# Kernel optimization log

Hardware: AMD Instinct MI355X
Metric: run time of the kernel (lower is better)

## Reference

```python
import jax, jax.numpy as jnp
import numpy as np

B, H, W = 8, 256, 256
NF = 64          # num_feat
E = 12           # num_expert
D = NF * 4       # token dim = 256
CD = D * E       # expanded dim = 3072


def _lrelu(x):
    return jnp.where(x >= 0, x, 0.2 * x)


def _conv(x, w, stride, pad):
    return jax.lax.conv_general_dilated(
        x, w, (stride, stride), [(pad, pad), (pad, pad)],
        dimension_numbers=('NCHW', 'OIHW', 'NCHW'))


def _bn(x, g, b):
    # training-mode BatchNorm2d: batch statistics over (N, H, W)
    m = jnp.mean(x, axis=(0, 2, 3), keepdims=True)
    v = jnp.var(x, axis=(0, 2, 3), keepdims=True)
    xn = (x - m) * jax.lax.rsqrt(v + 1e-5)
    return xn * g[None, :, None, None] + b[None, :, None, None]


def setup_inputs() -> dict:
    key = jax.random.key(0)
    ks = jax.random.split(key, 16)
    s = 0.05
    d = {}
    d['x'] = jax.random.normal(ks[0], (B, 3, H, W), jnp.float32)
    d['conv0_w'] = jax.random.normal(ks[1], (NF, 3, 3, 3)) * s
    d['conv0_b'] = jnp.zeros((NF,))
    d['conv1_w'] = jax.random.normal(ks[2], (NF, NF, 4, 4)) * s
    d['bn1_g'] = jnp.ones((NF,)); d['bn1_b'] = jnp.zeros((NF,))
    d['conv2_w'] = jax.random.normal(ks[3], (2 * NF, NF, 3, 3)) * s
    d['bn2_g'] = jnp.ones((2 * NF,)); d['bn2_b'] = jnp.zeros((2 * NF,))
    d['conv3_w'] = jax.random.normal(ks[4], (2 * NF, 2 * NF, 4, 4)) * s
    d['bn3_g'] = jnp.ones((2 * NF,)); d['bn3_b'] = jnp.zeros((2 * NF,))
    d['conv4_w'] = jax.random.normal(ks[5], (4 * NF, 2 * NF, 3, 3)) * s
    d['bn4_g'] = jnp.ones((4 * NF,)); d['bn4_b'] = jnp.zeros((4 * NF,))
    d['conv5_w'] = jax.random.normal(ks[6], (4 * NF, 4 * NF, 3, 3)) * s
    d['bn5_g'] = jnp.ones((4 * NF,)); d['bn5_b'] = jnp.zeros((4 * NF,))
    d['conv6_w'] = jax.random.normal(ks[7], (4 * NF, 4 * NF, 3, 3)) * s
    d['bn6_g'] = jnp.ones((4 * NF,)); d['bn6_b'] = jnp.zeros((4 * NF,))
    d['w_gating'] = jax.random.normal(ks[8], (D, E))          # torch.randn init
    d['body_w'] = jax.random.normal(ks[9], (D, CD)) * s       # Linear(c_dim, c_dim*blocks)
    d['body_b'] = jnp.zeros((CD,))
    d['ortho_w'] = jax.random.normal(ks[10], (1, 1, CD))      # OrthorTransform weight
    d['cls_w1'] = jax.random.normal(ks[11], (D, NF // 2)) * s # shared classifier
    d['cls_b1'] = jnp.zeros((NF // 2,))
    d['cls_w2'] = jax.random.normal(ks[12], (NF // 2, 1)) * s
    d['cls_b2'] = jnp.zeros((1,))
    return d


def reference(x, conv0_w, conv0_b, conv1_w, bn1_g, bn1_b, conv2_w, bn2_g, bn2_b,
              conv3_w, bn3_g, bn3_b, conv4_w, bn4_g, bn4_b, conv5_w, bn5_g, bn5_b,
              conv6_w, bn6_g, bn6_b, w_gating, body_w, body_b, ortho_w,
              cls_w1, cls_b1, cls_w2, cls_b2):
    # --- FE conv stack ---
    h = _lrelu(_conv(x, conv0_w, 1, 1) + conv0_b[None, :, None, None])
    h = _lrelu(_bn(_conv(h, conv1_w, 2, 1), bn1_g, bn1_b))
    h = _lrelu(_bn(_conv(h, conv2_w, 1, 1), bn2_g, bn2_b))
    h = _lrelu(_bn(_conv(h, conv3_w, 2, 1), bn3_g, bn3_b))
    h = _lrelu(_bn(_conv(h, conv4_w, 1, 1), bn4_g, bn4_b))
    h = _lrelu(_bn(_conv(h, conv5_w, 1, 1), bn5_g, bn5_b))
    h = _lrelu(_bn(_conv(h, conv6_w, 1, 1), bn6_g, bn6_b))
    b, c, hh, ww = h.shape
    tok = h.reshape(b, c, hh * ww).transpose(0, 2, 1)            # (B, N, D)
    # --- softmax router ---
    routing = jax.nn.softmax(jnp.einsum('bnd,de->bne', tok, w_gating), axis=-1)
    # --- CodeReduction: Linear + lrelu, OrthorTransform multiply, lrelu ---
    feat = _lrelu(tok @ body_w + body_b)                         # (B, N, E*D)
    feat = _lrelu(feat * ortho_w)
    feat = feat.reshape(b, hh * ww, E, D)                        # torch.split chunks
    # --- shared expert MLP on every chunk (all classifiers alias one module) ---
    hid = _lrelu(jnp.einsum('bned,df->bnef', feat, cls_w1) + cls_b1)
    outs = (jnp.einsum('bnef,fo->bneo', hid, cls_w2) + cls_b2)[..., 0]  # (B,N,E)
    # --- top-1 select (equivalent to the torch.where cascade) ---
    idx = jnp.argmax(routing, axis=-1, keepdims=True)
    output = jnp.take_along_axis(outs, idx, axis=-1)             # (B, N, 1)
    return output
```

## Files before the change

kernel.cpp:

```cpp
#include <hip/hip_runtime.h>

__device__ __forceinline__ float lrelu(float x) { return x >= 0.f ? x : 0.2f * x; }

typedef const __attribute__((address_space(1))) void* gas_ptr;
typedef __attribute__((address_space(3))) void* las_ptr;

__global__ __launch_bounds__(256) void conv0_k(const float* __restrict__ x,
                                               const float* __restrict__ w,
                                               const float* __restrict__ bias,
                                               float* __restrict__ out) {
    __shared__ float sIn[3][34][34];
    __shared__ float sW[27][16];
    const int H = 256;
    int tid = threadIdx.x, tx = tid & 31, ty = tid >> 5;
    int tX = (blockIdx.x & 7) * 32, tY = (blockIdx.x >> 3) * 32;
    int b = blockIdx.y, cog = blockIdx.z * 16;
    float acc[4][16] = {};
    const float* inB = x + (size_t)b * 3 * H * H;
    for (int idx = tid; idx < 3 * 1156; idx += 256) {
        int ci = idx / 1156, r = idx % 1156, iy = r / 34, ix = r % 34;
        int gy = tY - 1 + iy, gx = tX - 1 + ix;
        float v = 0.f;
        if ((unsigned)gy < 256u && (unsigned)gx < 256u)
            v = inB[(ci * H + gy) * H + gx];
        sIn[ci][iy][ix] = v;
    }
    for (int idx = tid; idx < 27 * 16; idx += 256) {
        int co = idx & 15, rest = idx >> 4;
        sW[rest][co] = w[(cog + co) * 27 + rest];
    }
    __syncthreads();
#pragma unroll
    for (int ci = 0; ci < 3; ci++)
#pragma unroll
        for (int dy = 0; dy < 3; dy++)
#pragma unroll
            for (int dx = 0; dx < 3; dx++) {
                float a0 = sIn[ci][ty + dy][tx + dx];
                float a1 = sIn[ci][ty + 8 + dy][tx + dx];
                float a2 = sIn[ci][ty + 16 + dy][tx + dx];
                float a3 = sIn[ci][ty + 24 + dy][tx + dx];
                const float* wp = sW[ci * 9 + dy * 3 + dx];
#pragma unroll
                for (int co = 0; co < 16; co++) {
                    float wv = wp[co];
                    acc[0][co] += a0 * wv; acc[1][co] += a1 * wv;
                    acc[2][co] += a2 * wv; acc[3][co] += a3 * wv;
                }
            }
    float* outB = out + (size_t)(b * 64 + cog) * 67080;
#pragma unroll
    for (int co = 0; co < 16; co++) {
        float bv = bias[cog + co];
#pragma unroll
        for (int r = 0; r < 4; r++)
            outB[(size_t)co * 67080 + (size_t)(tY + ty + 8 * r + 1) * 260 +
                 tX + tx + 1] = lrelu(acc[r][co] + bv);
    }
}

template <int COG, int RPT, int NWV>
__device__ __forceinline__ void stats_epi(float (&acc)[RPT][COG], float2* sRed,
                                          double2* part, int cog, int slotBase,
                                          int S, int tid) {
    const int lane = tid & 63, wv = tid >> 6;
    float s[COG], q[COG];
#pragma unroll
    for (int c = 0; c < COG; c++) {
        float ss = 0.f, qq = 0.f;
#pragma unroll
        for (int j = 0; j < RPT; j++) { float v = acc[j][c]; ss += v; qq += v * v; }
        s[c] = ss; q[c] = qq;
    }
#pragma unroll
    for (int off = 32; off; off >>= 1)
#pragma unroll
        for (int c = 0; c < COG; c++) {
            s[c] += __shfl_xor(s[c], off);
            q[c] += __shfl_xor(q[c], off);
        }
    if (lane == 0)
#pragma unroll
        for (int c = 0; c < COG; c++) sRed[wv * COG + c] = make_float2(s[c], q[c]);
    __syncthreads();
    if (tid < COG) {
        double ss = 0.0, qq = 0.0;
#pragma unroll
        for (int wvi = 0; wvi < NWV; wvi++) {
            float2 p = sRed[wvi * COG + tid];
            ss += (double)p.x; qq += (double)p.y;
        }
        int slot = slotBase + blockIdx.y * gridDim.x + blockIdx.x;
        part[(size_t)(cog + tid) * S + slot] = make_double2(ss, qq);
    }
}

template <int COG>
__global__ __launch_bounds__(128) void c4x4p_k(const float* __restrict__ in,
                                               const float* __restrict__ w,
                                               float* __restrict__ out,
                                               double2* __restrict__ part,
                                               int slotBase, int S,
                                               int Cin, int Cout, int Hin,
                                               int Hp, int Wp,
                                               int oHp, int oWp, int oOff) {
    constexpr int NSF4 = 34 * 17;
    constexpr int NR = (NSF4 + 127) / 128;
    __shared__ float sIn[2][34 * 68];
    __shared__ float sW[2][16 * COG];
    __shared__ float2 sRed[2 * COG];
    const int Hout = Hin >> 1;
    const int tid = threadIdx.x, tx = tid & 31, ty = tid >> 5;
    const int tpr = Hout >> 5;
    const int tX = (blockIdx.x % tpr) * 32, tY = (blockIdx.x / tpr) * 16;
    const int b = blockIdx.y, cog = blockIdx.z * COG;
    const int HWin = Hp * Wp;
    const float* inB = in + (size_t)b * Cin * HWin;
    const int wvbase = tid & ~63;

    int gOff[NR]; int lOff[NR]; bool act[NR];
#pragma unroll
    for (int r = 0; r < NR; r++) {
        int idx = tid + r * 128;
        bool a = idx < NSF4;
        int row = idx / 17, c4 = idx % 17;
        gOff[r] = a ? ((2 * tY + row) * Wp + 2 * tX + 4 * c4) : 0;
        lOff[r] = (r * 128 + wvbase) * 4;
        act[r] = a;
    }
    const int wco = tid % COG, wt = tid / COG;
    const int wgo = ((cog + wco) * Cin) * 16 + wt;

    float acc[4][COG];
#pragma unroll
    for (int j = 0; j < 4; j++)
#pragma unroll
        for (int c = 0; c < COG; c++) acc[j][c] = 0.f;

#pragma unroll
    for (int r = 0; r < NR; r++)
        if (act[r])
            __builtin_amdgcn_global_load_lds((gas_ptr)(inB + gOff[r]),
                                             (las_ptr)(&sIn[0][lOff[r]]), 16, 0, 0);
    __builtin_amdgcn_global_load_lds((gas_ptr)(w + wgo),
                                     (las_ptr)(&sW[0][wvbase]), 4, 0, 0);
    __syncthreads();

    for (int k = 0; k < Cin; k++) {
        const int cur = k & 1, nb = cur ^ 1;
        const bool more = (k + 1) < Cin;
        if (more) {
            const float* p = inB + (size_t)(k + 1) * HWin;
#pragma unroll
            for (int r = 0; r < NR; r++)
                if (act[r])
                    __builtin_amdgcn_global_load_lds(
                        (gas_ptr)(p + gOff[r]),
                        (las_ptr)(&sIn[nb][lOff[r]]), 16, 0, 0);
            __builtin_amdgcn_global_load_lds(
                (gas_ptr)(w + wgo + (k + 1) * 16),
                (las_ptr)(&sW[nb][wvbase]), 4, 0, 0);
        }
        const float* sI = sIn[cur];
        const float* sw = sW[cur];
#pragma unroll
        for (int dy = 0; dy < 4; dy++)
#pragma unroll
            for (int dx = 0; dx < 4; dx++) {
                const float* bp = sI + (2 * ty + dy) * 68 + 2 * tx + dx;
                float a0 = bp[0];
                float a1 = bp[8 * 68];
                float a2 = bp[16 * 68];
                float a3 = bp[24 * 68];
                const float* wp = sw + (dy * 4 + dx) * COG;
#pragma unroll
                for (int c = 0; c < COG; c++) {
                    float wv = wp[c];
                    acc[0][c] += a0 * wv; acc[1][c] += a1 * wv;
                    acc[2][c] += a2 * wv; acc[3][c] += a3 * wv;
                }
            }
        __syncthreads();
    }

    float* outB = out + (size_t)(b * Cout + cog) * oHp * oWp;
#pragma unroll
    for (int c = 0; c < COG; c++)
#pragma unroll
        for (int r = 0; r < 4; r++)
            outB[(size_t)c * oHp * oWp +
                 (size_t)(tY + ty + 4 * r + oOff) * oWp + tX + tx + oOff] =
                acc[r][c];
    stats_epi<COG, 4, 2>(acc, sRed, part, cog, slotBase, S, tid);
}

template <int COG>
__global__ __launch_bounds__(128) void c3x3_k(const float* __restrict__ in,
                                              const float* __restrict__ w,
                                              float* __restrict__ out,
                                              double2* __restrict__ part,
                                              int slotBase, int S,
                                              int Cin, int Cout, int H,
                                              int Hp, int Wp,
                                              int oHp, int oWp, int oOff) {
    constexpr int RS = 36;
    constexpr int ROWS = 34;
    constexpr int CI = ROWS * RS;
    constexpr int NSF4 = 2 * ROWS * 9;
    constexpr int NR = (NSF4 + 127) / 128;
    constexpr int NWR = (18 * COG + 127) / 128;
    __shared__ float sIn[2][2 * CI];
    __shared__ float sW[2][18 * COG];
    __shared__ float2 sRed[2 * COG];
    const int tid = threadIdx.x, tx = tid & 31, ty = tid >> 5;
    const int tpr = H >> 5;
    const int tX = (blockIdx.x % tpr) * 32, tY = (blockIdx.x / tpr) * 32;
    const int b = blockIdx.y, cog = blockIdx.z * COG;
    const int HWin = Hp * Wp;
    const float* inB = in + (size_t)b * Cin * HWin;
    const int wvbase = tid & ~63;

    int gOff[NR]; int lOff[NR]; bool act[NR];
#pragma unroll
    for (int r = 0; r < NR; r++) {
        int idx = tid + r * 128;
        bool a = idx < NSF4;
        int ci = idx / (9 * ROWS), rem = idx % (9 * ROWS);
        int row = rem / 9, c4 = rem % 9;
        gOff[r] = a ? (ci * HWin + (tY + row) * Wp + tX + 4 * c4) : 0;
        lOff[r] = (r * 128 + wvbase) * 4;
        act[r] = a;
    }
    int wgo[NWR]; bool wact[NWR]; int wlo[NWR];
#pragma unroll
    for (int r = 0; r < NWR; r++) {
        int widx = tid + r * 128;
        bool a = widx < 18 * COG;
        int co = widx % COG, rest = widx / COG;
        int ci = rest / 9, t = rest % 9;
        wgo[r] = a ? (((cog + co) * Cin + ci) * 9 + t) : 0;
        wlo[r] = r * 128 + wvbase;
        wact[r] = a;
    }

    float acc[8][COG];
#pragma unroll
    for (int j = 0; j < 8; j++)
#pragma unroll
        for (int c = 0; c < COG; c++) acc[j][c] = 0.f;

    const int steps = Cin >> 1;

    auto STAGE = [&](int t, int buf) {
        const float* p = inB + (size_t)(2 * t) * HWin;
#pragma unroll
        for (int r = 0; r < NR; r++)
            if (act[r])
                __builtin_amdgcn_global_load_lds(
                    (gas_ptr)(p + gOff[r]),
                    (las_ptr)(&sIn[buf][lOff[r]]), 16, 0, 0);
        const float* wp2 = w + (size_t)(2 * t) * 9;
#pragma unroll
        for (int r = 0; r < NWR; r++)
            if (wact[r])
                __builtin_amdgcn_global_load_lds(
                    (gas_ptr)(wp2 + wgo[r]),
                    (las_ptr)(&sW[buf][wlo[r]]), 4, 0, 0);
    };

    STAGE(0, 0);
    __syncthreads();
    for (int k = 0; k < steps; k++) {
        const int cur = k & 1, nb = cur ^ 1;
        if (k + 1 < steps) STAGE(k + 1, nb);
        const float* sI = sIn[cur];
        const float* sw = sW[cur];
#pragma unroll
        for (int ci = 0; ci < 2; ci++)
#pragma unroll
            for (int dx = 0; dx < 3; dx++) {
                const float* bp = sI + ci * CI + (8 * ty) * RS + tx + dx;
                float a[10];
#pragma unroll
                for (int j = 0; j < 10; j++) a[j] = bp[j * RS];
#pragma unroll
                for (int dy = 0; dy < 3; dy++) {
                    const float* wp = sw + (ci * 9 + dy * 3 + dx) * COG;
#pragma unroll
                    for (int c = 0; c < COG; c++) {
                        float wv = wp[c];
#pragma unroll
                        for (int j = 0; j < 8; j++)
                            acc[j][c] += a[j + dy] * wv;
                    }
                }
            }
        __syncthreads();
    }

    float* outB = out + (size_t)(b * Cout + cog) * oHp * oWp;
#pragma unroll
    for (int c = 0; c < COG; c++)
#pragma unroll
        for (int j = 0; j < 8; j++)
            outB[(size_t)c * oHp * oWp +
                 (size_t)(tY + 8 * ty + j + oOff) * oWp + tX + tx + oOff] =
                acc[j][c];
    stats_epi<COG, 8, 2>(acc, sRed, part, cog, slotBase, S, tid);
}

__global__ void bnfin_k(const double2* __restrict__ part, int S, int C, double invN,
                        const float* __restrict__ g, const float* __restrict__ bb,
                        float2* __restrict__ ss) {
    int c = threadIdx.x;
    if (c >= C) return;
    double sum = 0.0, sq = 0.0;
    for (int s = 0; s < S; s++) {
        double2 p = part[(size_t)c * S + s];
        sum += p.x; sq += p.y;
    }
    double m = sum * invN;
    double v = sq * invN - m * m;
    double sc = (double)g[c] / sqrt(v + 1e-5);
    ss[c] = make_float2((float)sc, (float)((double)bb[c] - m * sc));
}

__global__ __launch_bounds__(256) void bnact_k(float* __restrict__ p,
                                               const float2* __restrict__ ss,
                                               int C, int H, int W,
                                               int Hp, int Wp) {
    int pc = blockIdx.x;
    int c = pc & (C - 1);
    float2 t = ss ? ss[c] : make_float2(1.f, 0.f);
    bool xf = (ss != nullptr);
    float* pl = p + (size_t)pc * Hp * Wp;
    int n = Hp * Wp;
    for (int i = threadIdx.x; i < n; i += 256) {
        int y = i / Wp, x = i - y * Wp;
        bool inter = (y >= 1) && (y <= H) && (x >= 1) && (x <= W);
        if (!inter) pl[i] = 0.f;
        else if (xf) { float v = pl[i]; pl[i] = lrelu(t.x * v + t.y); }
    }
}

__global__ __launch_bounds__(256) void transp_k(const float* __restrict__ h6,
                                                const float2* __restrict__ ss,
                                                float* __restrict__ tok) {
    __shared__ float sT[32][33];
    int tx = threadIdx.x & 31, ty = threadIdx.x >> 5;
    int n0 = blockIdx.x * 32, d0 = blockIdx.y * 32, b = blockIdx.z;
    const float* hb = h6 + ((size_t)b * 256 + d0) * 4096 + n0;
#pragma unroll
    for (int r = 0; r < 4; r++) {
        int d = ty + 8 * r;
        float2 t = ss[d0 + d];
        sT[d][tx] = lrelu(t.x * hb[d * 4096 + tx] + t.y);
    }
    __syncthreads();
    float* tb = tok + ((size_t)b * 4096 + n0) * 256 + d0;
#pragma unroll
    for (int r = 0; r < 4; r++) {
        int n = ty + 8 * r;
        tb[n * 256 + tx] = sT[tx][n];
    }
}

__global__ __launch_bounds__(256) void token_k(const float* __restrict__ tok,
                                               const float* __restrict__ wg,
                                               const float* __restrict__ bw,
                                               const float* __restrict__ bb,
                                               const float* __restrict__ ow,
                                               const float* __restrict__ w1,
                                               const float* __restrict__ b1,
                                               const float* __restrict__ w2,
                                               const float* __restrict__ b2,
                                               float* __restrict__ outp) {
    __shared__ float sf[4][256];
    const int tid = threadIdx.x, wave = tid >> 6, l = tid & 63;
    const int t = blockIdx.x * 4 + wave;
    const float4 tv = reinterpret_cast<const float4*>(tok + (size_t)t * 256)[l];
    sf[wave][4 * l + 0] = tv.x; sf[wave][4 * l + 1] = tv.y;
    sf[wave][4 * l + 2] = tv.z; sf[wave][4 * l + 3] = tv.w;

    float lg[12];
#pragma unroll
    for (int e = 0; e < 12; e++) lg[e] = 0.f;
    const float tj[4] = {tv.x, tv.y, tv.z, tv.w};
#pragma unroll
    for (int j = 0; j < 4; j++) {
        const float* wr = wg + (4 * l + j) * 12;
#pragma unroll
        for (int e = 0; e < 12; e++) lg[e] += tj[j] * wr[e];
    }
#pragma unroll
    for (int off = 32; off > 0; off >>= 1) {
#pragma unroll
        for (int e = 0; e < 12; e++) lg[e] += __shfl_xor(lg[e], off);
    }
    int idx = 0; float best = lg[0];
#pragma unroll
    for (int e = 1; e < 12; e++)
        if (lg[e] > best) { best = lg[e]; idx = e; }
    const int cb = idx * 256;

    float f0 = 0.f, f1 = 0.f, f2 = 0.f, f3 = 0.f;
    const float* bwp = bw + cb + 4 * l;
#pragma unroll 4
    for (int d = 0; d < 256; d++) {
        const float td = sf[wave][d];
        const float4 wv = *reinterpret_cast<const float4*>(bwp + (size_t)d * 3072);
        f0 += td * wv.x; f1 += td * wv.y;
        f2 += td * wv.z; f3 += td * wv.w;
    }
    float fj[4] = {f0, f1, f2, f3};
#pragma unroll
    for (int j = 0; j < 4; j++) {
        int jj = cb + 4 * l + j;
        float v = lrelu(fj[j] + bb[jj]);
        v = lrelu(v * ow[jj]);
        sf[wave][4 * l + j] = v;
    }

    float o = 0.f;
    if (l < 32) {
        float h = b1[l];
#pragma unroll 4
        for (int j = 0; j < 256; j++) h += sf[wave][j] * w1[j * 32 + l];
        h = lrelu(h);
        o = h * w2[l];
    }
    o += __shfl_xor(o, 16); o += __shfl_xor(o, 8); o += __shfl_xor(o, 4);
    o += __shfl_xor(o, 2);  o += __shfl_xor(o, 1);
    if (l == 0) outp[t] = o + b2[0];
}

extern "C" void kernel_launch(void* const* d_in, const int* in_sizes, int n_in,
                              void* d_out, int out_size, void* d_ws, size_t ws_size,
                              hipStream_t stream) {
    const float* x   = (const float*)d_in[0];
    const float* w0  = (const float*)d_in[1];
    const float* b0  = (const float*)d_in[2];
    const float* w1  = (const float*)d_in[3];
    const float* g1  = (const float*)d_in[4];
    const float* be1 = (const float*)d_in[5];
    const float* w2  = (const float*)d_in[6];
    const float* g2  = (const float*)d_in[7];
    const float* be2 = (const float*)d_in[8];
    const float* w3  = (const float*)d_in[9];
    const float* g3  = (const float*)d_in[10];
    const float* be3 = (const float*)d_in[11];
    const float* w4  = (const float*)d_in[12];
    const float* g4  = (const float*)d_in[13];
    const float* be4 = (const float*)d_in[14];
    const float* w5  = (const float*)d_in[15];
    const float* g5  = (const float*)d_in[16];
    const float* be5 = (const float*)d_in[17];
    const float* w6  = (const float*)d_in[18];
    const float* g6  = (const float*)d_in[19];
    const float* be6 = (const float*)d_in[20];
    const float* wg  = (const float*)d_in[21];
    const float* bw  = (const float*)d_in[22];
    const float* bbp = (const float*)d_in[23];
    const float* owp = (const float*)d_in[24];
    const float* cw1 = (const float*)d_in[25];
    const float* cb1 = (const float*)d_in[26];
    const float* cw2 = (const float*)d_in[27];
    const float* cb2 = (const float*)d_in[28];

    char* W = (char*)d_ws;
    float2* ssb = (float2*)W;
    float2* ss1 = ssb;
    float2* ss2 = ssb + 64;
    float2* ss3 = ssb + 192;
    float2* ss4 = ssb + 320;
    float2* ss5 = ssb + 576;
    float2* ss6 = ssb + 832;
    double2* part = (double2*)(W + 16384);

    char* BIG = W + 278528;
    float* h0p = (float*)(BIG);
    float* h1p = (float*)(BIG + 70287360);
    float* h2p = (float*)(BIG);
    float* h3p = (float*)(BIG + 70287360);
    float* h4p = (float*)(BIG);
    float* h5p = (float*)(BIG + 36765696);
    float* h6  = (float*)(BIG);
    float* tok = (float*)(BIG + 36765696);

    bnact_k<<<256, 256, 0, stream>>>(h0p, nullptr, 64, 256, 256, 258, 260);
    for (int half = 0; half < 2; half++) {
        conv0_k<<<dim3(64, 4, 4), 256, 0, stream>>>(
            x + (size_t)half * 4 * 3 * 65536, w0, b0, h0p);
        c4x4p_k<8><<<dim3(32, 4, 8), 128, 0, stream>>>(
            h0p, w1, h1p + (size_t)half * 4 * 64 * 17160, part, half * 128, 256,
            64, 64, 256, 258, 260, 130, 132, 1);
    }
    bnfin_k<<<1, 256, 0, stream>>>(part, 256, 64, 1.0 / 131072.0, g1, be1, ss1);
    bnact_k<<<512, 256, 0, stream>>>(h1p, ss1, 64, 128, 128, 130, 132);
    c3x3_k<8><<<dim3(16, 8, 16), 128, 0, stream>>>(
        h1p, w2, h2p, part, 0, 128, 64, 128, 128, 130, 132, 130, 132, 1);
    bnfin_k<<<1, 256, 0, stream>>>(part, 128, 128, 1.0 / 131072.0, g2, be2, ss2);
    bnact_k<<<1024, 256, 0, stream>>>(h2p, ss2, 128, 128, 128, 130, 132);
    c4x4p_k<8><<<dim3(8, 8, 16), 128, 0, stream>>>(
        h2p, w3, h3p, part, 0, 64, 128, 128, 128, 130, 132, 66, 68, 1);
    bnfin_k<<<1, 256, 0, stream>>>(part, 64, 128, 1.0 / 32768.0, g3, be3, ss3);
    bnact_k<<<1024, 256, 0, stream>>>(h3p, ss3, 128, 64, 64, 66, 68);
    c3x3_k<8><<<dim3(4, 8, 32), 128, 0, stream>>>(
        h3p, w4, h4p, part, 0, 32, 128, 256, 64, 66, 68, 66, 68, 1);
    bnfin_k<<<1, 256, 0, stream>>>(part, 32, 256, 1.0 / 32768.0, g4, be4, ss4);
    bnact_k<<<2048, 256, 0, stream>>>(h4p, ss4, 256, 64, 64, 66, 68);
    c3x3_k<8><<<dim3(4, 8, 32), 128, 0, stream>>>(
        h4p, w5, h5p, part, 0, 32, 256, 256, 64, 66, 68, 66, 68, 1);
    bnfin_k<<<1, 256, 0, stream>>>(part, 32, 256, 1.0 / 32768.0, g5, be5, ss5);
    bnact_k<<<2048, 256, 0, stream>>>(h5p, ss5, 256, 64, 64, 66, 68);
    c3x3_k<8><<<dim3(4, 8, 32), 128, 0, stream>>>(
        h5p, w6, h6, part, 0, 32, 256, 256, 64, 66, 68, 64, 64, 0);
    bnfin_k<<<1, 256, 0, stream>>>(part, 32, 256, 1.0 / 32768.0, g6, be6, ss6);
    transp_k<<<dim3(128, 8, 8), 256, 0, stream>>>(h6, ss6, tok);
    token_k<<<8192, 256, 0, stream>>>(tok, wg, bw, bbp, owp, cw1, cb1, cw2, cb2,
                                      (float*)d_out);
}
```

Measured before the change: 2.550 ms.

## Use 4x2 register tiles in 3x3 conv and parallelize BN finalize per channel

The 3x3 conv thread mapping changes from 8 rows x 1 column per thread to 4 rows x 2 columns. Each thread now loads a 6x4 input window with float2 shared-memory reads and reuses it across all 9 taps, instead of reloading 10 values for each dx. This is meant to cut LDS traffic per FMA. Separately, the BN finalize kernel now launches one block per channel and reduces the partial sums with wave shuffles, replacing a single block that looped serially over all slots. The new output pixel ordering must stay consistent with stats_epi, which receives the same acc layout, and the wider register tile may raise register pressure.

Result: slower. 2.654 ms (+4.0%).

```diff
diff --git a/kernel.cpp b/kernel.cpp
--- a/kernel.cpp
+++ b/kernel.cpp
@@ -212,7 +212,8 @@
     __shared__ float sIn[2][2 * CI];
     __shared__ float sW[2][18 * COG];
     __shared__ float2 sRed[2 * COG];
-    const int tid = threadIdx.x, tx = tid & 31, ty = tid >> 5;
+    const int tid = threadIdx.x;
+    const int g = tid & 15, ty8 = tid >> 4;
     const int tpr = H >> 5;
     const int tX = (blockIdx.x % tpr) * 32, tY = (blockIdx.x / tpr) * 32;
     const int b = blockIdx.y, cog = blockIdx.z * COG;
@@ -276,25 +277,32 @@
         const float* sI = sIn[cur];
         const float* sw = sW[cur];
 #pragma unroll
-        for (int ci = 0; ci < 2; ci++)
-#pragma unroll
-            for (int dx = 0; dx < 3; dx++) {
-                const float* bp = sI + ci * CI + (8 * ty) * RS + tx + dx;
-                float a[10];
-#pragma unroll
-                for (int j = 0; j < 10; j++) a[j] = bp[j * RS];
-#pragma unroll
-                for (int dy = 0; dy < 3; dy++) {
+        for (int ci = 0; ci < 2; ci++) {
+            const float* bp = sI + ci * CI + (4 * ty8) * RS + 2 * g;
+            float a[6][4];
+#pragma unroll
+            for (int j = 0; j < 6; j++) {
+                float2 q0 = *(const float2*)(bp + j * RS);
+                float2 q1 = *(const float2*)(bp + j * RS + 2);
+                a[j][0] = q0.x; a[j][1] = q0.y;
+                a[j][2] = q1.x; a[j][3] = q1.y;
+            }
+#pragma unroll
+            for (int dy = 0; dy < 3; dy++)
+#pragma unroll
+                for (int dx = 0; dx < 3; dx++) {
                     const float* wp = sw + (ci * 9 + dy * 3 + dx) * COG;
 #pragma unroll
                     for (int c = 0; c < COG; c++) {
                         float wv = wp[c];
 #pragma unroll
-                        for (int j = 0; j < 8; j++)
-                            acc[j][c] += a[j + dy] * wv;
+                        for (int j = 0; j < 4; j++) {
+                            acc[j * 2 + 0][c] += a[j + dy][0 + dx] * wv;
+                            acc[j * 2 + 1][c] += a[j + dy][1 + dx] * wv;
+                        }
                     }
                 }
-            }
+        }
         __syncthreads();
     }
 
@@ -302,27 +310,43 @@
 #pragma unroll
     for (int c = 0; c < COG; c++)
 #pragma unroll
-        for (int j = 0; j < 8; j++)
-            outB[(size_t)c * oHp * oWp +
-                 (size_t)(tY + 8 * ty + j + oOff) * oWp + tX + tx + oOff] =
-                acc[j][c];
+        for (int j = 0; j < 4; j++)
+#pragma unroll
+            for (int cc = 0; cc < 2; cc++)
+                outB[(size_t)c * oHp * oWp +
+                     (size_t)(tY + 4 * ty8 + j + oOff) * oWp +
+                     tX + 2 * g + cc + oOff] = acc[j * 2 + cc][c];
     stats_epi<COG, 8, 2>(acc, sRed, part, cog, slotBase, S, tid);
 }
 
-__global__ void bnfin_k(const double2* __restrict__ part, int S, int C, double invN,
-                        const float* __restrict__ g, const float* __restrict__ bb,
-                        float2* __restrict__ ss) {
-    int c = threadIdx.x;
-    if (c >= C) return;
+__global__ __launch_bounds__(256) void bnfin_k(const double2* __restrict__ part,
+                                               int S, int C, double invN,
+                                               const float* __restrict__ g,
+                                               const float* __restrict__ bb,
+                                               float2* __restrict__ ss) {
+    __shared__ double2 red[4];
+    const int c = blockIdx.x, tid = threadIdx.x;
     double sum = 0.0, sq = 0.0;
-    for (int s = 0; s < S; s++) {
+    for (int s = tid; s < S; s += 256) {
         double2 p = part[(size_t)c * S + s];
         sum += p.x; sq += p.y;
     }
-    double m = sum * invN;
-    double v = sq * invN - m * m;
-    double sc = (double)g[c] / sqrt(v + 1e-5);
-    ss[c] = make_float2((float)sc, (float)((double)bb[c] - m * sc));
+#pragma unroll
+    for (int off = 32; off; off >>= 1) {
+        sum += __shfl_xor(sum, off);
+        sq += __shfl_xor(sq, off);
+    }
+    if ((tid & 63) == 0) red[tid >> 6] = make_double2(sum, sq);
+    __syncthreads();
+    if (tid == 0) {
+        double s2 = 0.0, q2 = 0.0;
+#pragma unroll
+        for (int wv = 0; wv < 4; wv++) { s2 += red[wv].x; q2 += red[wv].y; }
+        double m = s2 * invN;
+        double v = q2 * invN - m * m;
+        double sc = (double)g[c] / sqrt(v + 1e-5);
+        ss[c] = make_float2((float)sc, (float)((double)bb[c] - m * sc));
+    }
 }
 
 __global__ __launch_bounds__(256) void bnact_k(float* __restrict__ p,
@@ -495,27 +519,27 @@
             h0p, w1, h1p + (size_t)half * 4 * 64 * 17160, part, half * 128, 256,
             64, 64, 256, 258, 260, 130, 132, 1);
     }
-    bnfin_k<<<1, 256, 0, stream>>>(part, 256, 64, 1.0 / 131072.0, g1, be1, ss1);
+    bnfin_k<<<64, 256, 0, stream>>>(part, 256, 64, 1.0 / 131072.0, g1, be1, ss1);
     bnact_k<<<512, 256, 0, stream>>>(h1p, ss1, 64, 128, 128, 130, 132);
     c3x3_k<8><<<dim3(16, 8, 16), 128, 0, stream>>>(
         h1p, w2, h2p, part, 0, 128, 64, 128, 128, 130, 132, 130, 132, 1);
-    bnfin_k<<<1, 256, 0, stream>>>(part, 128, 128, 1.0 / 131072.0, g2, be2, ss2);
+    bnfin_k<<<128, 256, 0, stream>>>(part, 128, 128, 1.0 / 131072.0, g2, be2, ss2);
     bnact_k<<<1024, 256, 0, stream>>>(h2p, ss2, 128, 128, 128, 130, 132);
     c4x4p_k<8><<<dim3(8, 8, 16), 128, 0, stream>>>(
         h2p, w3, h3p, part, 0, 64, 128, 128, 128, 130, 132, 66, 68, 1);
-    bnfin_k<<<1, 256, 0, stream>>>(part, 64, 128, 1.0 / 32768.0, g3, be3, ss3);
+    bnfin_k<<<128, 256, 0, stream>>>(part, 64, 128, 1.0 / 32768.0, g3, be3, ss3);
     bnact_k<<<1024, 256, 0, stream>>>(h3p, ss3, 128, 64, 64, 66, 68);
     c3x3_k<8><<<dim3(4, 8, 32), 128, 0, stream>>>(
         h3p, w4, h4p, part, 0, 32, 128, 256, 64, 66, 68, 66, 68, 1);
-    bnfin_k<<<1, 256, 0, stream>>>(part, 32, 256, 1.0 / 32768.0, g4, be4, ss4);
+    bnfin_k<<<256, 256, 0, stream>>>(part, 32, 256, 1.0 / 32768.0, g4, be4, ss4);
     bnact_k<<<2048, 256, 0, stream>>>(h4p, ss4, 256, 64, 64, 66, 68);
     c3x3_k<8><<<dim3(4, 8, 32), 128, 0, stream>>>(
         h4p, w5, h5p, part, 0, 32, 256, 256, 64, 66, 68, 66, 68, 1);
-    bnfin_k<<<1, 256, 0, stream>>>(part, 32, 256, 1.0 / 32768.0, g5, be5, ss5);
+    bnfin_k<<<256, 256, 0, stream>>>(part, 32, 256, 1.0 / 32768.0, g5, be5, ss5);
     bnact_k<<<2048, 256, 0, stream>>>(h5p, ss5, 256, 64, 64, 66, 68);
     c3x3_k<8><<<dim3(4, 8, 32), 128, 0, stream>>>(
         h5p, w6, h6, part, 0, 32, 256, 256, 64, 66, 68, 64, 64, 0);
-    bnfin_k<<<1, 256, 0, stream>>>(part, 32, 256, 1.0 / 32768.0, g6, be6, ss6);
+    bnfin_k<<<256, 256, 0, stream>>>(part, 32, 256, 1.0 / 32768.0, g6, be6, ss6);
     transp_k<<<dim3(128, 8, 8), 256, 0, stream>>>(h6, ss6, tok);
     token_k<<<8192, 256, 0, stream>>>(tok, wg, bw, bbp, owp, cw1, cb1, cw2, cb2,
                                       (float*)d_out);
```
